# Kernel optimization log

Hardware: AMD Instinct MI355X
Metric: run time of the kernel (lower is better)

## Reference

```python
import jax, jax.numpy as jnp
import numpy as np

B, H, W, C1, C2 = 4, 256, 256, 256, 128
K = 128   # cells per patch (fixed for jit; original uses torch.unique)
E = 256   # emb_dim
NC = 16   # n_classes
G = 512   # n_genes
R = 64    # n_ref
HEADS = 8


def _w(k, shape):
    return jax.random.normal(k, shape, jnp.float32) / np.float32(np.sqrt(shape[-2]))


def setup_inputs() -> dict:
    key = jax.random.key(0)
    ks = jax.random.split(key, 20)
    return {
        "hd1": jax.random.normal(ks[0], (B, C1, H, W), jnp.float32),
        "h1": jax.random.normal(ks[1], (B, C2, H, W), jnp.float32),
        "ref_orig": jax.random.uniform(ks[2], (R, G), jnp.float32),
        "embed_w": _w(ks[3], (2 * (C1 + C2), E)),
        "comp_w1": _w(ks[4], (E, E)), "comp_w2": _w(ks[5], (E, NC)),
        "hist_w1": _w(ks[6], (E, E)), "hist_w2": _w(ks[7], (E, NC)),
        "genes_w1": _w(ks[8], (G, E)), "genes_w2": _w(ks[9], (E, NC)),
        "wref_w1": _w(ks[10], (3, E, E)), "wref_w2": _w(ks[11], (3, E, R)),
        "ca_wq": _w(ks[12], (3, NC, E)), "ca_wk": _w(ks[13], (3, G, E)),
        "ca_wv": _w(ks[14], (3, G, E)), "ca_wo": _w(ks[15], (3, E, G)),
        "nuclei_mask": jax.random.randint(ks[16], (B, H, W), 0, K + 1, jnp.int32),
        "n_cells": K,
    }


def _forward(hd1, h1, ref_orig, embed_w, comp_w1, comp_w2, hist_w1, hist_w2,
             genes_w1, genes_w2, wref_w1, wref_w2, ca_wq, ca_wk, ca_wv, ca_wo,
             nuclei_mask, n_cells):
    b, c1, hgt, wid = hd1.shape
    k_cells = n_cells
    # replaces the per-cell mask-multiply-sum loop with one segment reduce
    feat = jnp.concatenate([hd1, h1], axis=1)            # [B, C1+C2, H, W]
    cf = feat.shape[1]
    feat_flat = feat.transpose(0, 2, 3, 1).reshape(b * hgt * wid, cf)
    ids = nuclei_mask.reshape(b, hgt * wid)
    seg = jnp.where(ids > 0, jnp.arange(b)[:, None] * k_cells + ids - 1,
                    b * k_cells).reshape(-1)
    nseg = b * k_cells + 1                               # last bucket = background
    sums = jax.ops.segment_sum(feat_flat, seg, num_segments=nseg)[: b * k_cells]
    area = jax.ops.segment_sum(jnp.ones((seg.shape[0],), feat.dtype), seg,
                               num_segments=nseg)[: b * k_cells]
    cell_feat = sums / jnp.maximum(area, 1.0)[:, None]   # [N, Cf]
    glob = feat.mean((2, 3))                             # [B, Cf] = fv_hd1 ++ fv_h1
    all_fv = jnp.concatenate([cell_feat, jnp.repeat(glob, k_cells, axis=0)], axis=1)
    emb = all_fv @ embed_w                               # [N, E]
    emb_patches = emb.reshape(b, k_cells, -1).mean(1)    # per-patch mean embedding
    comp = jax.nn.softmax(jax.nn.relu(emb_patches @ comp_w1) @ comp_w2, axis=-1)
    comp_tiled = jnp.repeat(comp, k_cells, axis=0)       # [N, NC]
    out_cell_type = jax.nn.relu(emb @ hist_w1) @ hist_w2

    def branch(w1, w2, wq, wk, wv, wo):
        rw = jax.nn.softmax(jax.nn.relu(emb @ w1) @ w2, axis=-1)   # [N, R]
        ref_weighted = rw @ ref_orig                               # [N, G]
        dh = wq.shape[1] // HEADS
        q = (comp_tiled @ wq).reshape(-1, HEADS, dh)
        k = (ref_weighted @ wk).reshape(-1, HEADS, dh)
        v = (ref_weighted @ wv).reshape(-1, HEADS, dh)
        attn = jax.nn.softmax(jnp.einsum("qhd,khd->hqk", q, k) / float(np.sqrt(dh)), axis=-1)
        o = jnp.einsum("hqk,khd->qhd", attn, v).reshape(-1, HEADS * dh)
        return jax.nn.relu(ref_weighted + o @ wo)

    out_exprs = jax.vmap(branch)(wref_w1, wref_w2, ca_wq, ca_wk, ca_wv, ca_wo)  # [3,N,G]
    genes_h = jax.nn.relu(out_exprs[0] @ genes_w1)
    out_cell_type_expr = genes_h @ genes_w2
    return out_cell_type, out_exprs, out_cell_type_expr, genes_h, comp, area


def reference(hd1, h1, ref_orig, embed_w, comp_w1, comp_w2, hist_w1, hist_w2,
              genes_w1, genes_w2, wref_w1, wref_w2, ca_wq, ca_wk, ca_wv, ca_wo,
              nuclei_mask, n_cells):
    out_cell_type, out_exprs, out_cell_type_expr, genes_h, comp, area = _forward(
        hd1, h1, ref_orig, embed_w, comp_w1, comp_w2, hist_w1, hist_w2,
        genes_w1, genes_w2, wref_w1, wref_w2, ca_wq, ca_wk, ca_wv, ca_wo,
        nuclei_mask, n_cells)
    return (out_cell_type, out_exprs[0], out_exprs[1], out_exprs[2],
            out_cell_type_expr, genes_h, comp, area)
```

## Files before the change

### kernel.cpp

```cpp
#include <hip/hip_runtime.h>
#include <hip/hip_bf16.h>

#define Bn 4
#define C1n 256
#define C2n 128
#define CF 384
#define HWn 65536
#define Kc 128
#define Nn 512
#define En 256
#define NCn 16
#define Gn 512
#define Rn 64
#define HEADSn 8
#define DHn 32

#define CHK 32
#define PCH2 (HWn/CHK)
#define TC2 32
#define NT 64

#define SCALE_F 1048576.0f
#define INV_SCALE (1.0f/1048576.0f)

typedef unsigned long long ull;

__global__ __launch_bounds__(256) void area_k(const int* __restrict__ mask,
                                              int* __restrict__ apart) {
    int chunk = blockIdx.x, b = blockIdx.y;
    __shared__ int hist[4][129];
    int t = threadIdx.x, w = t >> 6;
    for (int i = t; i < 4 * 129; i += 256) ((int*)hist)[i] = 0;
    __syncthreads();
    const int* mp = mask + (size_t)b * HWn + chunk * PCH2;
    #pragma unroll
    for (int it = 0; it < PCH2 / 1024; ++it) {
        int4 v = *(const int4*)(mp + it * 1024 + t * 4);
        atomicAdd(&hist[w][v.x], 1);
        atomicAdd(&hist[w][v.y], 1);
        atomicAdd(&hist[w][v.z], 1);
        atomicAdd(&hist[w][v.w], 1);
    }
    __syncthreads();
    if (t < 128)
        apart[(chunk * Bn + b) * Kc + t] =
            hist[0][t+1] + hist[1][t+1] + hist[2][t+1] + hist[3][t+1];
}

__global__ __launch_bounds__(256) void segreduce3_k(
        const float* __restrict__ hd1, const float* __restrict__ h1,
        const int* __restrict__ mask,
        int* __restrict__ spart) {
    int chunk = blockIdx.x, cg = blockIdx.y, b = blockIdx.z;
    int c0 = cg * TC2;
    const float* base = (c0 < C1n)
        ? hd1 + ((size_t)(b * C1n + c0)) * HWn
        : h1  + ((size_t)(b * C2n + (c0 - C1n))) * HWn;
    const int* mp = mask + (size_t)b * HWn + chunk * PCH2;

    __shared__ int bins[129 * TC2];
    __shared__ float tile[NT * 33];
    __shared__ __align__(16) int idsh[NT];

    int t = threadIdx.x;
    int cL = t >> 3, l8 = t & 7;
    int cA = t & 31, pg = t >> 5;
    for (int i = t; i < 129 * TC2; i += 256) bins[i] = 0;
    __syncthreads();

    for (int tl = 0; tl < PCH2 / NT; ++tl) {
        int px0 = tl * NT;
        float4 v0 = *(const float4*)(base + (size_t)cL * HWn + px0 + l8 * 4);
        float4 v1 = *(const float4*)(base + (size_t)cL * HWn + px0 + 32 + l8 * 4);
        if (t < 16) *(int4*)&idsh[t * 4] = *(const int4*)(mp + px0 + t * 4);
        int p0 = l8 * 4;
        tile[(p0 + 0) * 33 + cL] = v0.x;
        tile[(p0 + 1) * 33 + cL] = v0.y;
        tile[(p0 + 2) * 33 + cL] = v0.z;
        tile[(p0 + 3) * 33 + cL] = v0.w;
        tile[(32 + p0 + 0) * 33 + cL] = v1.x;
        tile[(32 + p0 + 1) * 33 + cL] = v1.y;
        tile[(32 + p0 + 2) * 33 + cL] = v1.z;
        tile[(32 + p0 + 3) * 33 + cL] = v1.w;
        __syncthreads();
        #pragma unroll
        for (int pp = 0; pp < 8; ++pp) {
            int p = pg * 8 + pp;
            int id = idsh[p];
            float v = tile[p * 33 + cA];
            int qv = __float2int_rn(v * SCALE_F);
            atomicAdd(&bins[id * TC2 + cA], qv);
        }
        __syncthreads();
    }
    for (int i = t; i < 129 * TC2; i += 256) {
        int cell = i >> 5, cc = i & 31;
        spart[((size_t)(chunk * Bn + b) * 129 + cell) * CF + c0 + cc] = bins[i];
    }
}

__global__ void reduce_k(const int* __restrict__ spart, float* __restrict__ ctot) {
    int idx = blockIdx.x * 256 + threadIdx.x;
    if (idx >= Bn * 129 * CF) return;
    int b = idx / (129 * CF);
    int rem = idx - b * 129 * CF;
    long long s = 0;
    #pragma unroll 8
    for (int ch = 0; ch < CHK; ++ch)
        s += spart[((size_t)ch * Bn + b) * (129 * CF) + rem];
    ctot[idx] = (float)s * INV_SCALE;
}

__global__ void glob_k(const float* __restrict__ ctot, const int* __restrict__ apart,
                       float* __restrict__ glob,
                       float* __restrict__ areaf, float* __restrict__ area_out) {
    int idx = blockIdx.x * 256 + threadIdx.x;
    if (idx < Bn * CF) {
        int b = idx / CF, c = idx - b * CF;
        float s = 0.f;
        for (int cell = 0; cell < 129; ++cell)
            s += ctot[((size_t)(b * 129 + cell)) * CF + c];
        glob[idx] = s * (1.0f / (float)HWn);
    }
    if (idx < Nn) {
        int b = idx >> 7, cell = idx & 127;
        int s = 0;
        #pragma unroll 8
        for (int ch = 0; ch < CHK; ++ch)
            s += apart[(ch * Bn + b) * Kc + cell];
        float a = (float)s;
        areaf[idx] = a;
        area_out[idx] = a;
    }
}

__global__ __launch_bounds__(256) void gemm_emb_k(
        const float* __restrict__ ctot, const float* __restrict__ glob,
        const float* __restrict__ areaf, const float* __restrict__ Bw,
        float* __restrict__ C) {
    int row0 = blockIdx.x * 2;
    __shared__ float As[2 * 768];
    __shared__ float part[2048];
    __shared__ float rina[2];
    int t = threadIdx.x, lane = t & 63, w = t >> 6;
    if (t < 2) rina[t] = 1.f / fmaxf(areaf[row0 + t], 1.f);
    __syncthreads();
    for (int idx = t; idx < 2 * 768; idx += 256) {
        int r = idx / 768, k = idx - r * 768;
        int row = row0 + r;
        float v;
        if (k < CF) {
            int bb = row >> 7, cell = (row & 127) + 1;
            v = ctot[((size_t)(bb * 129 + cell)) * CF + k] * rina[r];
        } else {
            v = glob[(row >> 7) * CF + (k - CF)];
        }
        As[idx] = v;
    }
    __syncthreads();
    float acc[2][4] = {{0,0,0,0},{0,0,0,0}};
    const int KQ = 192;
    const float* bp = Bw + (size_t)(w * KQ) * 256 + lane * 4;
    #pragma unroll 8
    for (int k = 0; k < KQ; ++k) {
        float4 bv = *(const float4*)(bp + (size_t)k * 256);
        float a0 = As[w * KQ + k], a1 = As[768 + w * KQ + k];
        acc[0][0] = fmaf(a0, bv.x, acc[0][0]); acc[0][1] = fmaf(a0, bv.y, acc[0][1]);
        acc[0][2] = fmaf(a0, bv.z, acc[0][2]); acc[0][3] = fmaf(a0, bv.w, acc[0][3]);
        acc[1][0] = fmaf(a1, bv.x, acc[1][0]); acc[1][1] = fmaf(a1, bv.y, acc[1][1]);
        acc[1][2] = fmaf(a1, bv.z, acc[1][2]); acc[1][3] = fmaf(a1, bv.w, acc[1][3]);
    }
    *(float4*)&part[(w * 2 + 0) * 256 + lane * 4] = make_float4(acc[0][0], acc[0][1], acc[0][2], acc[0][3]);
    *(float4*)&part[(w * 2 + 1) * 256 + lane * 4] = make_float4(acc[1][0], acc[1][1], acc[1][2], acc[1][3]);
    __syncthreads();
    #pragma unroll
    for (int i2 = 0; i2 < 2; ++i2) {
        int idx = i2 * 256 + t, r = idx >> 8, c = idx & 255;
        float s = part[r*256+c] + part[(2+r)*256+c] + part[(4+r)*256+c] + part[(6+r)*256+c];
        C[(size_t)(row0 + r) * En + c] = s;
    }
}

__global__ void patch_mean_k(const float* __restrict__ emb, float* __restrict__ ep) {
    int b = blockIdx.x, j = threadIdx.x;
    float s = 0.f;
    for (int r = 0; r < Kc; r++) s += emb[(size_t)(b * Kc + r) * En + j];
    ep[b * En + j] = s * (1.f / (float)Kc);
}

__global__ void comp_mlp_k(const float* __restrict__ ep, const float* __restrict__ w1,
                           const float* __restrict__ w2, float* __restrict__ comp_ws,
                           float* __restrict__ comp_out) {
    int b = blockIdx.x, j = threadIdx.x;
    __shared__ float h[En];
    __shared__ float c[NCn];
    float acc = 0.f;
    #pragma unroll 8
    for (int k = 0; k < En; k++) acc = fmaf(ep[b * En + k], w1[(size_t)k * En + j], acc);
    h[j] = fmaxf(acc, 0.f);
    __syncthreads();
    if (j < NCn) {
        float a2 = 0.f;
        #pragma unroll 8
        for (int k = 0; k < En; k++) a2 = fmaf(h[k], w2[(size_t)k * NCn + j], a2);
        c[j] = a2;
    }
    __syncthreads();
    if (j == 0) {
        float m = c[0];
        for (int q = 1; q < NCn; q++) m = fmaxf(m, c[q]);
        float s = 0.f;
        for (int q = 0; q < NCn; q++) { c[q] = __expf(c[q] - m); s += c[q]; }
        float inv = 1.f / s;
        for (int q = 0; q < NCn; q++) c[q] *= inv;
    }
    __syncthreads();
    if (j < NCn) {
        comp_ws[b * NCn + j] = c[j];
        comp_out[b * NCn + j] = c[j];
    }
}

__global__ __launch_bounds__(256) void fused_hist_k(
        const float* __restrict__ emb, const float* __restrict__ w1,
        const float* __restrict__ w2, float* __restrict__ out) {
    int row0 = blockIdx.x * 2;
    __shared__ float As[2 * En];
    __shared__ float part[2048];
    __shared__ float Hs[2 * En];
    int t = threadIdx.x, lane = t & 63, w = t >> 6;
    if (t < 128) *(float4*)&As[t * 4] = *(const float4*)(emb + (size_t)row0 * En + t * 4);
    __syncthreads();
    float acc[2][4] = {{0,0,0,0},{0,0,0,0}};
    const float* bp = w1 + (size_t)(w * 64) * 256 + lane * 4;
    #pragma unroll 8
    for (int k = 0; k < 64; ++k) {
        float4 bv = *(const float4*)(bp + (size_t)k * 256);
        float a0 = As[w * 64 + k], a1 = As[256 + w * 64 + k];
        acc[0][0] = fmaf(a0, bv.x, acc[0][0]); acc[0][1] = fmaf(a0, bv.y, acc[0][1]);
        acc[0][2] = fmaf(a0, bv.z, acc[0][2]); acc[0][3] = fmaf(a0, bv.w, acc[0][3]);
        acc[1][0] = fmaf(a1, bv.x, acc[1][0]); acc[1][1] = fmaf(a1, bv.y, acc[1][1]);
        acc[1][2] = fmaf(a1, bv.z, acc[1][2]); acc[1][3] = fmaf(a1, bv.w, acc[1][3]);
    }
    *(float4*)&part[(w * 2 + 0) * 256 + lane * 4] = make_float4(acc[0][0], acc[0][1], acc[0][2], acc[0][3]);
    *(float4*)&part[(w * 2 + 1) * 256 + lane * 4] = make_float4(acc[1][0], acc[1][1], acc[1][2], acc[1][3]);
    __syncthreads();
    #pragma unroll
    for (int i2 = 0; i2 < 2; ++i2) {
        int idx = i2 * 256 + t, r = idx >> 8, c = idx & 255;
        float s = part[r*256+c] + part[(2+r)*256+c] + part[(4+r)*256+c] + part[(6+r)*256+c];
        Hs[r * 256 + c] = fmaxf(s, 0.f);
    }
    __syncthreads();
    if (t < 32) {
        int r = t >> 4, j = t & 15;
        float a2 = 0.f;
        #pragma unroll 8
        for (int k = 0; k < En; k++) a2 = fmaf(Hs[r * 256 + k], w2[(size_t)k * NCn + j], a2);
        out[(size_t)(row0 + r) * NCn + j] = a2;
    }
}

__global__ __launch_bounds__(256) void fused_branch_k(
        const float* __restrict__ emb, const float* __restrict__ wref_w1,
        const float* __restrict__ wref_w2, const float* __restrict__ ref,
        float* __restrict__ refw) {
    int i = blockIdx.y, row0 = blockIdx.x * 2;
    const float* w1 = wref_w1 + (size_t)i * En * En;
    const float* w2 = wref_w2 + (size_t)i * En * Rn;
    __shared__ float As[2 * En];
    __shared__ float part[2048];
    __shared__ float Hs[2 * En];
    __shared__ float RW[2 * Rn];
    int t = threadIdx.x, lane = t & 63, w = t >> 6;
    if (t < 128) *(float4*)&As[t * 4] = *(const float4*)(emb + (size_t)row0 * En + t * 4);
    __syncthreads();
    {
        float acc[2][4] = {{0,0,0,0},{0,0,0,0}};
        const float* bp = w1 + (size_t)(w * 64) * 256 + lane * 4;
        #pragma unroll 8
        for (int k = 0; k < 64; ++k) {
            float4 bv = *(const float4*)(bp + (size_t)k * 256);
            float a0 = As[w * 64 + k], a1 = As[256 + w * 64 + k];
            acc[0][0] = fmaf(a0, bv.x, acc[0][0]); acc[0][1] = fmaf(a0, bv.y, acc[0][1]);
            acc[0][2] = fmaf(a0, bv.z, acc[0][2]); acc[0][3] = fmaf(a0, bv.w, acc[0][3]);
            acc[1][0] = fmaf(a1, bv.x, acc[1][0]); acc[1][1] = fmaf(a1, bv.y, acc[1][1]);
            acc[1][2] = fmaf(a1, bv.z, acc[1][2]); acc[1][3] = fmaf(a1, bv.w, acc[1][3]);
        }
        *(float4*)&part[(w * 2 + 0) * 256 + lane * 4] = make_float4(acc[0][0], acc[0][1], acc[0][2], acc[0][3]);
        *(float4*)&part[(w * 2 + 1) * 256 + lane * 4] = make_float4(acc[1][0], acc[1][1], acc[1][2], acc[1][3]);
    }
    __syncthreads();
    #pragma unroll
    for (int i2 = 0; i2 < 2; ++i2) {
        int idx = i2 * 256 + t, r = idx >> 8, c = idx & 255;
        float s = part[r*256+c] + part[(2+r)*256+c] + part[(4+r)*256+c] + part[(6+r)*256+c];
        Hs[r * 256 + c] = fmaxf(s, 0.f);
    }
    __syncthreads();
    {
        float a0 = 0.f, a1 = 0.f;
        const float* bp = w2 + (size_t)(w * 64) * 64 + lane;
        #pragma unroll 8
        for (int k = 0; k < 64; ++k) {
            float bv = bp[(size_t)k * 64];
            a0 = fmaf(Hs[w * 64 + k], bv, a0);
            a1 = fmaf(Hs[256 + w * 64 + k], bv, a1);
        }
        part[(w * 2 + 0) * 64 + lane] = a0;
        part[(w * 2 + 1) * 64 + lane] = a1;
    }
    __syncthreads();
    if (t < 128) {
        int r = t >> 6, c = t & 63;
        RW[r * 64 + c] = part[r*64+c] + part[(2+r)*64+c] + part[(4+r)*64+c] + part[(6+r)*64+c];
    }
    __syncthreads();
    if (w < 2) {
        float v = RW[w * 64 + lane];
        float m = v;
        #pragma unroll
        for (int o = 32; o > 0; o >>= 1) m = fmaxf(m, __shfl_xor(m, o));
        float e = __expf(v - m), s = e;
        #pragma unroll
        for (int o = 32; o > 0; o >>= 1) s += __shfl_xor(s, o);
        RW[w * 64 + lane] = e / s;
    }
    __syncthreads();
    {
        int q = t & 127, kh = t >> 7;
        float acc[2][4] = {{0,0,0,0},{0,0,0,0}};
        const float* bp = ref + (size_t)(kh * 32) * 512 + q * 4;
        #pragma unroll 8
        for (int k = 0; k < 32; ++k) {
            float4 bv = *(const float4*)(bp + (size_t)k * 512);
            float a0 = RW[kh * 32 + k], a1 = RW[64 + kh * 32 + k];
            acc[0][0] = fmaf(a0, bv.x, acc[0][0]); acc[0][1] = fmaf(a0, bv.y, acc[0][1]);
            acc[0][2] = fmaf(a0, bv.z, acc[0][2]); acc[0][3] = fmaf(a0, bv.w, acc[0][3]);
            acc[1][0] = fmaf(a1, bv.x, acc[1][0]); acc[1][1] = fmaf(a1, bv.y, acc[1][1]);
            acc[1][2] = fmaf(a1, bv.z, acc[1][2]); acc[1][3] = fmaf(a1, bv.w, acc[1][3]);
        }
        *(float4*)&part[(kh * 2 + 0) * 512 + q * 4] = make_float4(acc[0][0], acc[0][1], acc[0][2], acc[0][3]);
        *(float4*)&part[(kh * 2 + 1) * 512 + q * 4] = make_float4(acc[1][0], acc[1][1], acc[1][2], acc[1][3]);
    }
    __syncthreads();
    float* op = refw + ((size_t)i * Nn + row0) * Gn;
    #pragma unroll
    for (int i2 = 0; i2 < 4; ++i2) {
        int idx = i2 * 256 + t, r = idx >> 9, c = idx & 511;
        op[(size_t)r * Gn + c] = part[r * 512 + c] + part[(2 + r) * 512 + c];
    }
}

__global__ __launch_bounds__(256) void fused_kv_k(
        const float* __restrict__ refw, const float* __restrict__ ca_wk,
        const float* __restrict__ ca_wv, float* __restrict__ kws,
        float* __restrict__ vws) {
    int i = blockIdx.y, row0 = blockIdx.x * 2;
    const float* wk = ca_wk + (size_t)i * Gn * En;
    const float* wv = ca_wv + (size_t)i * Gn * En;
    __shared__ float As[2 * Gn];
    __shared__ float part[2048];
    int t = threadIdx.x, lane = t & 63, w = t >> 6;
    const float* rp = refw + ((size_t)i * Nn + row0) * Gn;
    *(float4*)&As[t * 4] = *(const float4*)(rp + t * 4);
    __syncthreads();
    int which = w >> 1, half = w & 1;
    const float* Bp = (which ? wv : wk) + (size_t)(half * 256) * En + lane * 4;
    float acc[2][4] = {{0,0,0,0},{0,0,0,0}};
    #pragma unroll 8
    for (int k = 0; k < 256; ++k) {
        float4 bv = *(const float4*)(Bp + (size_t)k * En);
        float a0 = As[half * 256 + k], a1 = As[512 + half * 256 + k];
        acc[0][0] = fmaf(a0, bv.x, acc[0][0]); acc[0][1] = fmaf(a0, bv.y, acc[0][1]);
        acc[0][2] = fmaf(a0, bv.z, acc[0][2]); acc[0][3] = fmaf(a0, bv.w, acc[0][3]);
        acc[1][0] = fmaf(a1, bv.x, acc[1][0]); acc[1][1] = fmaf(a1, bv.y, acc[1][1]);
        acc[1][2] = fmaf(a1, bv.z, acc[1][2]); acc[1][3] = fmaf(a1, bv.w, acc[1][3]);
    }
    *(float4*)&part[(w * 2 + 0) * 256 + lane * 4] = make_float4(acc[0][0], acc[0][1], acc[0][2], acc[0][3]);
    *(float4*)&part[(w * 2 + 1) * 256 + lane * 4] = make_float4(acc[1][0], acc[1][1], acc[1][2], acc[1][3]);
    __syncthreads();
    #pragma unroll
    for (int i2 = 0; i2 < 2; ++i2) {
        int idx = i2 * 256 + t, r = idx >> 8, c = idx & 255;
        float sk = part[r * 256 + c] + part[(2 + r) * 256 + c];
        float sv = part[(4 + r) * 256 + c] + part[(6 + r) * 256 + c];
        kws[((size_t)i * Nn + row0 + r) * En + c] = sk;
        vws[((size_t)i * Nn + row0 + r) * En + c] = sv;
    }
}

template <int R, bool RELU>
__global__ void gemm_rows_k(const float* __restrict__ A, long long sA,
                            const float* __restrict__ Bw, long long sB,
                            float* __restrict__ C, long long sC,
                            int M, int N, int K) {
    int i = blockIdx.y;
    A += (size_t)i * sA; Bw += (size_t)i * sB; C += (size_t)i * sC;
    int row0 = blockIdx.x * R;
    extern __shared__ float As[];
    for (int idx = threadIdx.x; idx < R * K; idx += blockDim.x)
        As[idx] = A[(size_t)(row0 + idx / K) * K + (idx % K)];
    __syncthreads();
    for (int j = threadIdx.x; j < N; j += blockDim.x) {
        float acc[R];
        #pragma unroll
        for (int r = 0; r < R; r++) acc[r] = 0.f;
        const float* bp = Bw + j;
        #pragma unroll 8
        for (int k = 0; k < K; k++) {
            float bv = bp[(size_t)k * N];
            #pragma unroll
            for (int r = 0; r < R; r++) acc[r] = fmaf(As[r * K + k], bv, acc[r]);
        }
        #pragma unroll
        for (int r = 0; r < R; r++) {
            float v = acc[r];
            if (RELU) v = fmaxf(v, 0.f);
            C[(size_t)(row0 + r) * N + j] = v;
        }
    }
}

__global__ __launch_bounds__(256) void attn_k(
        const float* __restrict__ compw, const float* __restrict__ wq,
        const float* __restrict__ kmat, const float* __restrict__ vmat,
        float* __restrict__ o4) {
    int i = blockIdx.y, b = blockIdx.x & 3, h = blockIdx.x >> 2;
    const float* wqi = wq + (size_t)i * NCn * En;
    const float* km = kmat + (size_t)i * Nn * En;
    const float* vm = vmat + (size_t)i * Nn * En;
    __shared__ float q[DHn];
    __shared__ float p[Nn];
    __shared__ float red[4];
    __shared__ float pvp[8][33];
    int t = threadIdx.x;
    if (t < DHn) {
        float acc = 0.f;
        #pragma unroll
        for (int c = 0; c < NCn; c++)
            acc = fmaf(compw[b * NCn + c], wqi[(size_t)c * En + h * DHn + t], acc);
        q[t] = acc;
    }
    __syncthreads();
    const float scale = 0.17677669529663687f;
    float sv0, sv1;
    {
        const float* kr = km + (size_t)t * En + h * DHn;
        float a = 0.f;
        #pragma unroll
        for (int d = 0; d < DHn; d++) a = fmaf(q[d], kr[d], a);
        sv0 = a * scale;
        kr += (size_t)256 * En;
        a = 0.f;
        #pragma unroll
        for (int d = 0; d < DHn; d++) a = fmaf(q[d], kr[d], a);
        sv1 = a * scale;
    }
    float lm = fmaxf(sv0, sv1);
    #pragma unroll
    for (int o = 32; o > 0; o >>= 1) lm = fmaxf(lm, __shfl_xor(lm, o));
    if ((t & 63) == 0) red[t >> 6] = lm;
    __syncthreads();
    float m = fmaxf(fmaxf(red[0], red[1]), fmaxf(red[2], red[3]));
    __syncthreads();
    float e0 = __expf(sv0 - m), e1 = __expf(sv1 - m);
    p[t] = e0; p[t + 256] = e1;
    float ls = e0 + e1;
    #pragma unroll
    for (int o = 32; o > 0; o >>= 1) ls += __shfl_xor(ls, o);
    if ((t & 63) == 0) red[t >> 6] = ls;
    __syncthreads();
    float ssum = red[0] + red[1] + red[2] + red[3];
    int d = t & 31, seg = t >> 5;
    float acc = 0.f;
    const float* vp = vm + (size_t)(seg * 64) * En + h * DHn + d;
    #pragma unroll 8
    for (int j = 0; j < 64; ++j) acc = fmaf(p[seg * 64 + j], vp[(size_t)j * En], acc);
    pvp[seg][d] = acc;
    __syncthreads();
    if (t < DHn) {
        float o = 0.f;
        #pragma unroll
        for (int s8 = 0; s8 < 8; ++s8) o += pvp[s8][t];
        o4[((size_t)i * Bn + b) * En + h * DHn + t] = o / ssum;
    }
}

__global__ void add_relu_k(const float* __restrict__ refw, const float* __restrict__ ow,
                           float* __restrict__ out) {
    int i = blockIdx.y, n = blockIdx.x, b = n >> 7;
    const float4* rr = (const float4*)(refw + ((size_t)i * Nn + n) * Gn);
    const float4* oo = (const float4*)(ow + ((size_t)i * Bn + b) * Gn);
    float4* op = (float4*)(out + (size_t)i * (Nn * Gn) + (size_t)n * Gn);
    int j = threadIdx.x;
    float4 a = rr[j], o = oo[j];
    op[j] = make_float4(fmaxf(a.x + o.x, 0.f), fmaxf(a.y + o.y, 0.f),
                        fmaxf(a.z + o.z, 0.f), fmaxf(a.w + o.w, 0.f));
}

__global__ __launch_bounds__(256) void fused_genes_k(
        const float* __restrict__ e0, const float* __restrict__ gw1,
        const float* __restrict__ gw2, float* __restrict__ gh,
        float* __restrict__ octe) {
    int row0 = blockIdx.x * 2;
    __shared__ float As[2 * Gn];
    __shared__ float part[2048];
    __shared__ float Hs[2 * En];
    int t = threadIdx.x, lane = t & 63, w = t >> 6;
    *(float4*)&As[t * 4] = *(const float4*)(e0 + (size_t)row0 * Gn + t * 4);
    __syncthreads();
    {
        float acc[2][4] = {{0,0,0,0},{0,0,0,0}};
        const float* bp = gw1 + (size_t)(w * 128) * 256 + lane * 4;
        #pragma unroll 8
        for (int k = 0; k < 128; ++k) {
            float4 bv = *(const float4*)(bp + (size_t)k * 256);
            float a0 = As[w * 128 + k], a1 = As[512 + w * 128 + k];
            acc[0][0] = fmaf(a0, bv.x, acc[0][0]); acc[0][1] = fmaf(a0, bv.y, acc[0][1]);
            acc[0][2] = fmaf(a0, bv.z, acc[0][2]); acc[0][3] = fmaf(a0, bv.w, acc[0][3]);
            acc[1][0] = fmaf(a1, bv.x, acc[1][0]); acc[1][1] = fmaf(a1, bv.y, acc[1][1]);
            acc[1][2] = fmaf(a1, bv.z, acc[1][2]); acc[1][3] = fmaf(a1, bv.w, acc[1][3]);
        }
        *(float4*)&part[(w * 2 + 0) * 256 + lane * 4] = make_float4(acc[0][0], acc[0][1], acc[0][2], acc[0][3]);
        *(float4*)&part[(w * 2 + 1) * 256 + lane * 4] = make_float4(acc[1][0], acc[1][1], acc[1][2], acc[1][3]);
    }
    __syncthreads();
    #pragma unroll
    for (int i2 = 0; i2 < 2; ++i2) {
        int idx = i2 * 256 + t, r = idx >> 8, c = idx & 255;
        float s = part[r*256+c] + part[(2+r)*256+c] + part[(4+r)*256+c] + part[(6+r)*256+c];
        float v = fmaxf(s, 0.f);
        Hs[r * 256 + c] = v;
        gh[(size_t)(row0 + r) * En + c] = v;
    }
    __syncthreads();
    if (t < 32) {
        int r = t >> 4, j = t & 15;
        float a2 = 0.f;
        #pragma unroll 8
        for (int k = 0; k < En; k++) a2 = fmaf(Hs[r * 256 + k], gw2[(size_t)k * NCn + j], a2);
        octe[(size_t)(row0 + r) * NCn + j] = a2;
    }
}

extern "C" void kernel_launch(void* const* d_in, const int* in_sizes, int n_in,
                              void* d_out, int out_size, void* d_ws, size_t ws_size,
                              hipStream_t stream) {
    const float* hd1     = (const float*)d_in[0];
    const float* h1      = (const float*)d_in[1];
    const float* ref     = (const float*)d_in[2];
    const float* embed_w = (const float*)d_in[3];
    const float* comp_w1 = (const float*)d_in[4];
    const float* comp_w2 = (const float*)d_in[5];
    const float* hist_w1 = (const float*)d_in[6];
    const float* hist_w2 = (const float*)d_in[7];
    const float* genes_w1= (const float*)d_in[8];
    const float* genes_w2= (const float*)d_in[9];
    const float* wref_w1 = (const float*)d_in[10];
    const float* wref_w2 = (const float*)d_in[11];
    const float* ca_wq   = (const float*)d_in[12];
    const float* ca_wk   = (const float*)d_in[13];
    const float* ca_wv   = (const float*)d_in[14];
    const float* ca_wo   = (const float*)d_in[15];
    const int*   mask    = (const int*)d_in[16];

    float* out = (float*)d_out;
    const size_t o_ct   = 0;
    const size_t o_e0   = 8192;
    const size_t o_octe = 8192 + 3 * 262144;
    const size_t o_gh   = o_octe + 8192;
    const size_t o_comp = o_gh + 131072;
    const size_t o_area = o_comp + 64;

    int*  spart = (int*)d_ws;
    int*  apart = spart + (size_t)CHK * Bn * 129 * CF;
    float* ctot = (float*)(apart + CHK * Bn * Kc);
    float* glob = ctot + Bn * 129 * CF;
    float* areaf = glob + 1536;
    float* emb   = areaf + 512;
    float* ep    = emb + 131072;
    float* compw = ep + 1024;
    float* refw  = compw + 64;
    float* kws   = refw + 786432;
    float* vws   = kws + 393216;
    float* o4    = vws + 393216;
    float* ow    = o4 + 3072;

    area_k<<<dim3(CHK, Bn), 256, 0, stream>>>(mask, apart);
    segreduce3_k<<<dim3(CHK, CF / TC2, Bn), 256, 0, stream>>>(hd1, h1, mask, spart);
    reduce_k<<<(Bn * 129 * CF + 255) / 256, 256, 0, stream>>>(spart, ctot);
    glob_k<<<6, 256, 0, stream>>>(ctot, apart, glob, areaf, out + o_area);
    gemm_emb_k<<<Nn / 2, 256, 0, stream>>>(ctot, glob, areaf, embed_w, emb);
    patch_mean_k<<<Bn, 256, 0, stream>>>(emb, ep);
    comp_mlp_k<<<Bn, 256, 0, stream>>>(ep, comp_w1, comp_w2, compw, out + o_comp);

    fused_hist_k<<<Nn / 2, 256, 0, stream>>>(emb, hist_w1, hist_w2, out + o_ct);
    fused_branch_k<<<dim3(Nn / 2, 3), 256, 0, stream>>>(emb, wref_w1, wref_w2, ref, refw);
    fused_kv_k<<<dim3(Nn / 2, 3), 256, 0, stream>>>(refw, ca_wk, ca_wv, kws, vws);
    attn_k<<<dim3(HEADSn * Bn, 3), 256, 0, stream>>>(compw, ca_wq, kws, vws, o4);
    gemm_rows_k<4, false><<<dim3(1, 3), 256, 4 * 256 * 4, stream>>>(
        o4, (long long)Bn * En, ca_wo, (long long)En * Gn, ow, (long long)Bn * Gn, Bn, Gn, En);
    add_relu_k<<<dim3(Nn, 3), 128, 0, stream>>>(refw, ow, out + o_e0);

    fused_genes_k<<<Nn / 2, 256, 0, stream>>>(out + o_e0, genes_w1, genes_w2,
                                              out + o_gh, out + o_octe);
}
```

Before: 657.0 us.

## Drop LDS transpose in segreduce, raise row tiling in branch/kv kernels, fuse patch mean

The segment-reduce kernel no longer stages values through a shared transposed tile. Each thread now reads its channel row and mask ids directly and atomically adds into padded shared bins, which removes two barriers per tile. fused_branch_k processes 4 rows per block and fused_kv_k processes 8, so each weight load is reused across more rows, at the cost of more registers and shared memory. The patch-mean kernel is folded into comp_mlp_k, and the final wo GEMM is spread over more blocks. The trade-offs are more mask reloads per channel thread and possible occupancy loss in the bigger-tile kernels.

```diff
diff --git a/kernel.cpp b/kernel.cpp
--- a/kernel.cpp
+++ b/kernel.cpp
@@ -18,7 +18,6 @@
 #define CHK 32
 #define PCH2 (HWn/CHK)
 #define TC2 32
-#define NT 64
 
 #define SCALE_F 1048576.0f
 #define INV_SCALE (1.0f/1048576.0f)
@@ -58,44 +57,32 @@
         : h1  + ((size_t)(b * C2n + (c0 - C1n))) * HWn;
     const int* mp = mask + (size_t)b * HWn + chunk * PCH2;
 
-    __shared__ int bins[129 * TC2];
-    __shared__ float tile[NT * 33];
-    __shared__ __align__(16) int idsh[NT];
+    __shared__ int bins[129 * 33];
 
     int t = threadIdx.x;
     int cL = t >> 3, l8 = t & 7;
-    int cA = t & 31, pg = t >> 5;
-    for (int i = t; i < 129 * TC2; i += 256) bins[i] = 0;
-    __syncthreads();
-
-    for (int tl = 0; tl < PCH2 / NT; ++tl) {
-        int px0 = tl * NT;
-        float4 v0 = *(const float4*)(base + (size_t)cL * HWn + px0 + l8 * 4);
-        float4 v1 = *(const float4*)(base + (size_t)cL * HWn + px0 + 32 + l8 * 4);
-        if (t < 16) *(int4*)&idsh[t * 4] = *(const int4*)(mp + px0 + t * 4);
-        int p0 = l8 * 4;
-        tile[(p0 + 0) * 33 + cL] = v0.x;
-        tile[(p0 + 1) * 33 + cL] = v0.y;
-        tile[(p0 + 2) * 33 + cL] = v0.z;
-        tile[(p0 + 3) * 33 + cL] = v0.w;
-        tile[(32 + p0 + 0) * 33 + cL] = v1.x;
-        tile[(32 + p0 + 1) * 33 + cL] = v1.y;
-        tile[(32 + p0 + 2) * 33 + cL] = v1.z;
-        tile[(32 + p0 + 3) * 33 + cL] = v1.w;
-        __syncthreads();
-        #pragma unroll
-        for (int pp = 0; pp < 8; ++pp) {
-            int p = pg * 8 + pp;
-            int id = idsh[p];
-            float v = tile[p * 33 + cA];
-            int qv = __float2int_rn(v * SCALE_F);
-            atomicAdd(&bins[id * TC2 + cA], qv);
-        }
-        __syncthreads();
-    }
+    for (int i = t; i < 129 * 33; i += 256) bins[i] = 0;
+    __syncthreads();
+
+    const float* rowp = base + (size_t)cL * HWn;
+    for (int px0 = l8 * 4; px0 < PCH2; px0 += 64) {
+        float4 v0 = *(const float4*)(rowp + px0);
+        float4 v1 = *(const float4*)(rowp + px0 + 32);
+        int4 i0 = *(const int4*)(mp + px0);
+        int4 i1 = *(const int4*)(mp + px0 + 32);
+        atomicAdd(&bins[i0.x * 33 + cL], __float2int_rn(v0.x * SCALE_F));
+        atomicAdd(&bins[i0.y * 33 + cL], __float2int_rn(v0.y * SCALE_F));
+        atomicAdd(&bins[i0.z * 33 + cL], __float2int_rn(v0.z * SCALE_F));
+        atomicAdd(&bins[i0.w * 33 + cL], __float2int_rn(v0.w * SCALE_F));
+        atomicAdd(&bins[i1.x * 33 + cL], __float2int_rn(v1.x * SCALE_F));
+        atomicAdd(&bins[i1.y * 33 + cL], __float2int_rn(v1.y * SCALE_F));
+        atomicAdd(&bins[i1.z * 33 + cL], __float2int_rn(v1.z * SCALE_F));
+        atomicAdd(&bins[i1.w * 33 + cL], __float2int_rn(v1.w * SCALE_F));
+    }
+    __syncthreads();
     for (int i = t; i < 129 * TC2; i += 256) {
         int cell = i >> 5, cc = i & 31;
-        spart[((size_t)(chunk * Bn + b) * 129 + cell) * CF + c0 + cc] = bins[i];
+        spart[((size_t)(chunk * Bn + b) * 129 + cell) * CF + c0 + cc] = bins[cell * 33 + cc];
     }
 }
 
@@ -181,22 +168,20 @@
     }
 }
 
-__global__ void patch_mean_k(const float* __restrict__ emb, float* __restrict__ ep) {
-    int b = blockIdx.x, j = threadIdx.x;
-    float s = 0.f;
-    for (int r = 0; r < Kc; r++) s += emb[(size_t)(b * Kc + r) * En + j];
-    ep[b * En + j] = s * (1.f / (float)Kc);
-}
-
-__global__ void comp_mlp_k(const float* __restrict__ ep, const float* __restrict__ w1,
+__global__ void comp_mlp_k(const float* __restrict__ emb, const float* __restrict__ w1,
                            const float* __restrict__ w2, float* __restrict__ comp_ws,
                            float* __restrict__ comp_out) {
     int b = blockIdx.x, j = threadIdx.x;
+    __shared__ float eps[En];
     __shared__ float h[En];
     __shared__ float c[NCn];
+    float s0 = 0.f;
+    for (int r = 0; r < Kc; r++) s0 += emb[(size_t)(b * Kc + r) * En + j];
+    eps[j] = s0 * (1.f / (float)Kc);
+    __syncthreads();
     float acc = 0.f;
     #pragma unroll 8
-    for (int k = 0; k < En; k++) acc = fmaf(ep[b * En + k], w1[(size_t)k * En + j], acc);
+    for (int k = 0; k < En; k++) acc = fmaf(eps[k], w1[(size_t)k * En + j], acc);
     h[j] = fmaxf(acc, 0.f);
     __syncthreads();
     if (j < NCn) {
@@ -265,58 +250,61 @@
         const float* __restrict__ emb, const float* __restrict__ wref_w1,
         const float* __restrict__ wref_w2, const float* __restrict__ ref,
         float* __restrict__ refw) {
-    int i = blockIdx.y, row0 = blockIdx.x * 2;
+    int i = blockIdx.y, row0 = blockIdx.x * 4;
     const float* w1 = wref_w1 + (size_t)i * En * En;
     const float* w2 = wref_w2 + (size_t)i * En * Rn;
-    __shared__ float As[2 * En];
-    __shared__ float part[2048];
-    __shared__ float Hs[2 * En];
-    __shared__ float RW[2 * Rn];
+    __shared__ float As[4 * En];
+    __shared__ float part[4096];
+    __shared__ float Hs[4 * En];
+    __shared__ float RW[4 * Rn];
     int t = threadIdx.x, lane = t & 63, w = t >> 6;
-    if (t < 128) *(float4*)&As[t * 4] = *(const float4*)(emb + (size_t)row0 * En + t * 4);
+    *(float4*)&As[t * 4] = *(const float4*)(emb + (size_t)row0 * En + t * 4);
     __syncthreads();
     {
-        float acc[2][4] = {{0,0,0,0},{0,0,0,0}};
+        float acc[4][4] = {{0,0,0,0},{0,0,0,0},{0,0,0,0},{0,0,0,0}};
         const float* bp = w1 + (size_t)(w * 64) * 256 + lane * 4;
-        #pragma unroll 8
+        #pragma unroll 4
         for (int k = 0; k < 64; ++k) {
             float4 bv = *(const float4*)(bp + (size_t)k * 256);
-            float a0 = As[w * 64 + k], a1 = As[256 + w * 64 + k];
-            acc[0][0] = fmaf(a0, bv.x, acc[0][0]); acc[0][1] = fmaf(a0, bv.y, acc[0][1]);
-            acc[0][2] = fmaf(a0, bv.z, acc[0][2]); acc[0][3] = fmaf(a0, bv.w, acc[0][3]);
-            acc[1][0] = fmaf(a1, bv.x, acc[1][0]); acc[1][1] = fmaf(a1, bv.y, acc[1][1]);
-            acc[1][2] = fmaf(a1, bv.z, acc[1][2]); acc[1][3] = fmaf(a1, bv.w, acc[1][3]);
-        }
-        *(float4*)&part[(w * 2 + 0) * 256 + lane * 4] = make_float4(acc[0][0], acc[0][1], acc[0][2], acc[0][3]);
-        *(float4*)&part[(w * 2 + 1) * 256 + lane * 4] = make_float4(acc[1][0], acc[1][1], acc[1][2], acc[1][3]);
-    }
-    __syncthreads();
-    #pragma unroll
-    for (int i2 = 0; i2 < 2; ++i2) {
+            #pragma unroll
+            for (int r = 0; r < 4; ++r) {
+                float a = As[r * 256 + w * 64 + k];
+                acc[r][0] = fmaf(a, bv.x, acc[r][0]); acc[r][1] = fmaf(a, bv.y, acc[r][1]);
+                acc[r][2] = fmaf(a, bv.z, acc[r][2]); acc[r][3] = fmaf(a, bv.w, acc[r][3]);
+            }
+        }
+        #pragma unroll
+        for (int r = 0; r < 4; ++r)
+            *(float4*)&part[(w * 4 + r) * 256 + lane * 4] =
+                make_float4(acc[r][0], acc[r][1], acc[r][2], acc[r][3]);
+    }
+    __syncthreads();
+    #pragma unroll
+    for (int i2 = 0; i2 < 4; ++i2) {
         int idx = i2 * 256 + t, r = idx >> 8, c = idx & 255;
-        float s = part[r*256+c] + part[(2+r)*256+c] + part[(4+r)*256+c] + part[(6+r)*256+c];
+        float s = part[r*256+c] + part[(4+r)*256+c] + part[(8+r)*256+c] + part[(12+r)*256+c];
         Hs[r * 256 + c] = fmaxf(s, 0.f);
     }
     __syncthreads();
     {
-        float a0 = 0.f, a1 = 0.f;
+        float a[4] = {0.f, 0.f, 0.f, 0.f};
         const float* bp = w2 + (size_t)(w * 64) * 64 + lane;
         #pragma unroll 8
         for (int k = 0; k < 64; ++k) {
             float bv = bp[(size_t)k * 64];
-            a0 = fmaf(Hs[w * 64 + k], bv, a0);
-            a1 = fmaf(Hs[256 + w * 64 + k], bv, a1);
-        }
-        part[(w * 2 + 0) * 64 + lane] = a0;
-        part[(w * 2 + 1) * 64 + lane] = a1;
-    }
-    __syncthreads();
-    if (t < 128) {
+            #pragma unroll
+            for (int r = 0; r < 4; ++r) a[r] = fmaf(Hs[r * 256 + w * 64 + k], bv, a[r]);
+        }
+        #pragma unroll
+        for (int r = 0; r < 4; ++r) part[(w * 4 + r) * 64 + lane] = a[r];
+    }
+    __syncthreads();
+    {
         int r = t >> 6, c = t & 63;
-        RW[r * 64 + c] = part[r*64+c] + part[(2+r)*64+c] + part[(4+r)*64+c] + part[(6+r)*64+c];
-    }
-    __syncthreads();
-    if (w < 2) {
+        RW[r * 64 + c] = part[r*64+c] + part[(4+r)*64+c] + part[(8+r)*64+c] + part[(12+r)*64+c];
+    }
+    __syncthreads();
+    {
         float v = RW[w * 64 + lane];
         float m = v;
         #pragma unroll
@@ -329,26 +317,29 @@
     __syncthreads();
     {
         int q = t & 127, kh = t >> 7;
-        float acc[2][4] = {{0,0,0,0},{0,0,0,0}};
+        float acc[4][4] = {{0,0,0,0},{0,0,0,0},{0,0,0,0},{0,0,0,0}};
         const float* bp = ref + (size_t)(kh * 32) * 512 + q * 4;
-        #pragma unroll 8
+        #pragma unroll 4
         for (int k = 0; k < 32; ++k) {
             float4 bv = *(const float4*)(bp + (size_t)k * 512);
-            float a0 = RW[kh * 32 + k], a1 = RW[64 + kh * 32 + k];
-            acc[0][0] = fmaf(a0, bv.x, acc[0][0]); acc[0][1] = fmaf(a0, bv.y, acc[0][1]);
-            acc[0][2] = fmaf(a0, bv.z, acc[0][2]); acc[0][3] = fmaf(a0, bv.w, acc[0][3]);
-            acc[1][0] = fmaf(a1, bv.x, acc[1][0]); acc[1][1] = fmaf(a1, bv.y, acc[1][1]);
-            acc[1][2] = fmaf(a1, bv.z, acc[1][2]); acc[1][3] = fmaf(a1, bv.w, acc[1][3]);
-        }
-        *(float4*)&part[(kh * 2 + 0) * 512 + q * 4] = make_float4(acc[0][0], acc[0][1], acc[0][2], acc[0][3]);
-        *(float4*)&part[(kh * 2 + 1) * 512 + q * 4] = make_float4(acc[1][0], acc[1][1], acc[1][2], acc[1][3]);
+            #pragma unroll
+            for (int r = 0; r < 4; ++r) {
+                float a = RW[r * 64 + kh * 32 + k];
+                acc[r][0] = fmaf(a, bv.x, acc[r][0]); acc[r][1] = fmaf(a, bv.y, acc[r][1]);
+                acc[r][2] = fmaf(a, bv.z, acc[r][2]); acc[r][3] = fmaf(a, bv.w, acc[r][3]);
+            }
+        }
+        #pragma unroll
+        for (int r = 0; r < 4; ++r)
+            *(float4*)&part[(kh * 4 + r) * 512 + q * 4] =
+                make_float4(acc[r][0], acc[r][1], acc[r][2], acc[r][3]);
     }
     __syncthreads();
     float* op = refw + ((size_t)i * Nn + row0) * Gn;
     #pragma unroll
-    for (int i2 = 0; i2 < 4; ++i2) {
+    for (int i2 = 0; i2 < 8; ++i2) {
         int idx = i2 * 256 + t, r = idx >> 9, c = idx & 511;
-        op[(size_t)r * Gn + c] = part[r * 512 + c] + part[(2 + r) * 512 + c];
+        op[(size_t)r * Gn + c] = part[r * 512 + c] + part[(4 + r) * 512 + c];
     }
 }
 
@@ -356,35 +347,42 @@
         const float* __restrict__ refw, const float* __restrict__ ca_wk,
         const float* __restrict__ ca_wv, float* __restrict__ kws,
         float* __restrict__ vws) {
-    int i = blockIdx.y, row0 = blockIdx.x * 2;
+    int i = blockIdx.y, row0 = blockIdx.x * 8;
     const float* wk = ca_wk + (size_t)i * Gn * En;
     const float* wv = ca_wv + (size_t)i * Gn * En;
-    __shared__ float As[2 * Gn];
-    __shared__ float part[2048];
+    __shared__ float As[8 * Gn];
+    __shared__ float part[8192];
     int t = threadIdx.x, lane = t & 63, w = t >> 6;
     const float* rp = refw + ((size_t)i * Nn + row0) * Gn;
-    *(float4*)&As[t * 4] = *(const float4*)(rp + t * 4);
+    #pragma unroll
+    for (int q = 0; q < 4; ++q)
+        *(float4*)&As[q * 1024 + t * 4] = *(const float4*)(rp + q * 1024 + t * 4);
     __syncthreads();
     int which = w >> 1, half = w & 1;
     const float* Bp = (which ? wv : wk) + (size_t)(half * 256) * En + lane * 4;
-    float acc[2][4] = {{0,0,0,0},{0,0,0,0}};
-    #pragma unroll 8
+    float acc[8][4];
+    #pragma unroll
+    for (int r = 0; r < 8; ++r) { acc[r][0]=0.f; acc[r][1]=0.f; acc[r][2]=0.f; acc[r][3]=0.f; }
+    #pragma unroll 4
     for (int k = 0; k < 256; ++k) {
         float4 bv = *(const float4*)(Bp + (size_t)k * En);
-        float a0 = As[half * 256 + k], a1 = As[512 + half * 256 + k];
-        acc[0][0] = fmaf(a0, bv.x, acc[0][0]); acc[0][1] = fmaf(a0, bv.y, acc[0][1]);
-        acc[0][2] = fmaf(a0, bv.z, acc[0][2]); acc[0][3] = fmaf(a0, bv.w, acc[0][3]);
-        acc[1][0] = fmaf(a1, bv.x, acc[1][0]); acc[1][1] = fmaf(a1, bv.y, acc[1][1]);
-        acc[1][2] = fmaf(a1, bv.z, acc[1][2]); acc[1][3] = fmaf(a1, bv.w, acc[1][3]);
-    }
-    *(float4*)&part[(w * 2 + 0) * 256 + lane * 4] = make_float4(acc[0][0], acc[0][1], acc[0][2], acc[0][3]);
-    *(float4*)&part[(w * 2 + 1) * 256 + lane * 4] = make_float4(acc[1][0], acc[1][1], acc[1][2], acc[1][3]);
-    __syncthreads();
-    #pragma unroll
-    for (int i2 = 0; i2 < 2; ++i2) {
+        #pragma unroll
+        for (int r = 0; r < 8; ++r) {
+            float a = As[r * 512 + half * 256 + k];
+            acc[r][0] = fmaf(a, bv.x, acc[r][0]); acc[r][1] = fmaf(a, bv.y, acc[r][1]);
+            acc[r][2] = fmaf(a, bv.z, acc[r][2]); acc[r][3] = fmaf(a, bv.w, acc[r][3]);
+        }
+    }
+    #pragma unroll
+    for (int r = 0; r < 8; ++r)
+        *(float4*)&part[(w * 8 + r) * 256 + lane * 4] =
+            make_float4(acc[r][0], acc[r][1], acc[r][2], acc[r][3]);
+    __syncthreads();
+    #pragma unroll
+    for (int i2 = 0; i2 < 8; ++i2) {
         int idx = i2 * 256 + t, r = idx >> 8, c = idx & 255;
-        float sk = part[r * 256 + c] + part[(2 + r) * 256 + c];
-        float sv = part[(4 + r) * 256 + c] + part[(6 + r) * 256 + c];
+        float sk = part[r * 256 + c] + part[(8 + r) * 256 + c];
+        float sv = part[(16 + r) * 256 + c] + part[(24 + r) * 256 + c];
         kws[((size_t)i * Nn + row0 + r) * En + c] = sk;
         vws[((size_t)i * Nn + row0 + r) * En + c] = sv;
     }
@@ -579,8 +577,7 @@
     float* glob = ctot + Bn * 129 * CF;
     float* areaf = glob + 1536;
     float* emb   = areaf + 512;
-    float* ep    = emb + 131072;
-    float* compw = ep + 1024;
+    float* compw = emb + 131072;
     float* refw  = compw + 64;
     float* kws   = refw + 786432;
     float* vws   = kws + 393216;
@@ -592,14 +589,13 @@
     reduce_k<<<(Bn * 129 * CF + 255) / 256, 256, 0, stream>>>(spart, ctot);
     glob_k<<<6, 256, 0, stream>>>(ctot, apart, glob, areaf, out + o_area);
     gemm_emb_k<<<Nn / 2, 256, 0, stream>>>(ctot, glob, areaf, embed_w, emb);
-    patch_mean_k<<<Bn, 256, 0, stream>>>(emb, ep);
-    comp_mlp_k<<<Bn, 256, 0, stream>>>(ep, comp_w1, comp_w2, compw, out + o_comp);
+    comp_mlp_k<<<Bn, 256, 0, stream>>>(emb, comp_w1, comp_w2, compw, out + o_comp);
 
     fused_hist_k<<<Nn / 2, 256, 0, stream>>>(emb, hist_w1, hist_w2, out + o_ct);
-    fused_branch_k<<<dim3(Nn / 2, 3), 256, 0, stream>>>(emb, wref_w1, wref_w2, ref, refw);
-    fused_kv_k<<<dim3(Nn / 2, 3), 256, 0, stream>>>(refw, ca_wk, ca_wv, kws, vws);
+    fused_branch_k<<<dim3(Nn / 4, 3), 256, 0, stream>>>(emb, wref_w1, wref_w2, ref, refw);
+    fused_kv_k<<<dim3(Nn / 8, 3), 256, 0, stream>>>(refw, ca_wk, ca_wv, kws, vws);
     attn_k<<<dim3(HEADSn * Bn, 3), 256, 0, stream>>>(compw, ca_wq, kws, vws, o4);
-    gemm_rows_k<4, false><<<dim3(1, 3), 256, 4 * 256 * 4, stream>>>(
+    gemm_rows_k<1, false><<<dim3(Bn, 3), 256, 256 * 4, stream>>>(
         o4, (long long)Bn * En, ca_wo, (long long)En * Gn, ow, (long long)Bn * Gn, Bn, Gn, En);
     add_relu_k<<<dim3(Nn, 3), 128, 0, stream>>>(refw, ow, out + o_e0);
 
```

Result: no change. 646.9 us (-1.5%).
